# Kernel optimization log

Hardware: AMD Instinct MI355X
Metric: run time of the kernel (lower is better)

The kernel has to match this reference:

```python
import jax, jax.numpy as jnp
import numpy as np
from math import sqrt

B, TS_D, SEG, D, H = 16, 2, 1024, 256, 8
D_FF = 1024
DK = D // H
EPS = 1e-5


def _layernorm(x, g, b):
    mu = jnp.mean(x, axis=-1, keepdims=True)
    var = jnp.mean(jnp.square(x - mu), axis=-1, keepdims=True)
    return (x - mu) * jax.lax.rsqrt(var + EPS) * g + b


def setup_inputs() -> dict:
    key = jax.random.key(0)
    ks = jax.random.split(key, 16)
    s = 0.02
    return {
        "x": jax.random.normal(ks[0], (B, TS_D, SEG, D), dtype=jnp.float32),
        "Wq": jax.random.normal(ks[1], (D, D), dtype=jnp.float32) * s,
        "bq": jnp.zeros((D,), jnp.float32),
        "Wk": jax.random.normal(ks[2], (D, D), dtype=jnp.float32) * s,
        "bk": jnp.zeros((D,), jnp.float32),
        "Wv": jax.random.normal(ks[3], (D, D), dtype=jnp.float32) * s,
        "bv": jnp.zeros((D,), jnp.float32),
        "Wo": jax.random.normal(ks[4], (D, D), dtype=jnp.float32) * s,
        "bo": jnp.zeros((D,), jnp.float32),
        "g31": jnp.ones((D,), jnp.float32),
        "b31": jnp.zeros((D,), jnp.float32),
        "W1": jax.random.normal(ks[5], (D, D_FF), dtype=jnp.float32) * s,
        "b1": jnp.zeros((D_FF,), jnp.float32),
        "W2": jax.random.normal(ks[6], (D_FF, D), dtype=jnp.float32) * s,
        "b2": jnp.zeros((D,), jnp.float32),
        "g41": jnp.ones((D,), jnp.float32),
        "b41": jnp.zeros((D,), jnp.float32),
    }


def reference(x, Wq, bq, Wk, bk, Wv, bv, Wo, bo, g31, b31, W1, b1, W2, b2, g41, b41):
    # x: [B, ts_d=2, seg, d]; output is final_out2 (only live path of the module)
    b, ts_d, seg, d = x.shape
    scale = 1.0 / sqrt(DK)
    segments = x.reshape(b, ts_d * seg, d)            # [B, 2*seg, d]
    Q = (segments @ Wq + bq).reshape(b, -1, H, DK)
    K = (segments @ Wk + bk).reshape(b, -1, H, DK)
    V = (segments @ Wv + bv).reshape(b, -1, H, DK)
    q = Q[:, :seg]       # first seg positions (channel 0)
    k = K[:, -seg:]      # last seg positions (channel 1)
    v = V[:, -seg:]
    # cross-segment dual attention
    A1 = jax.nn.softmax(scale * jnp.einsum('blhe,bshe->bhls', q, k), axis=-1)
    out1 = jnp.einsum('bhls,bshd->blhd', A1, v).reshape(b, seg, d)
    A2 = jax.nn.softmax(scale * jnp.einsum('blhe,bshe->bhls', k, q), axis=-1)
    out2 = jnp.einsum('bhls,bshd->blhd', A2, q).reshape(b, seg, d)
    y = jnp.concatenate([out1, out2], axis=1) @ Wo + bo   # [B, 2*seg, d]
    h = _layernorm(segments + y, g31, b31)
    mlp = jax.nn.gelu(h @ W1 + b1, approximate=False) @ W2 + b2
    h = _layernorm(h + mlp, g41, b41)
    return h.reshape(b, ts_d, seg, d)
```

## Files before the change

kernel.cpp:

```cpp
#include <hip/hip_runtime.h>
#include <hip/hip_bf16.h>
#include <math.h>

#define BATCH 16
#define SEG 1024
#define DMODEL 256
#define NH 8
#define DK 32
#define DFF 1024
#define NTOK (BATCH * 2 * SEG)
#define EPS 1e-5f

typedef __attribute__((ext_vector_type(8))) short short8;
typedef __attribute__((ext_vector_type(4))) short short4b;
typedef __attribute__((ext_vector_type(4))) float f32x4;

#if __has_builtin(__builtin_amdgcn_exp2f)
#define EXP2(x) __builtin_amdgcn_exp2f(x)
#else
#define EXP2(x) __expf((x) * 0.6931471805599453f)
#endif

__device__ __forceinline__ ushort f2bf(float x) {
    union { float f; unsigned u; } a; a.f = x;
    unsigned r = a.u + 0x7fffu + ((a.u >> 16) & 1u);
    return (ushort)(r >> 16);
}

typedef const __attribute__((address_space(1))) unsigned gas_u32;
typedef __attribute__((address_space(3))) unsigned las_u32;
__device__ __forceinline__ void gload_lds16(const ushort* g, ushort* l) {
    __builtin_amdgcn_global_load_lds((gas_u32*)g, (las_u32*)l, 16, 0, 0);
}

__global__ __launch_bounds__(256) void wfrag_kernel(
    const float* __restrict__ src, ushort* __restrict__ dst, int K, int N, int order)
{
    const int tid = blockIdx.x * 256 + threadIdx.x;
    const int KT_ = K >> 5, NT_ = N >> 4;
    const int total = KT_ * NT_ * 64;
    if (tid >= total) return;
    const int lane = tid & 63;
    const int frag = tid >> 6;
    int kt, nt;
    if (order) { kt = frag / NT_; nt = frag % NT_; }
    else       { nt = frag / KT_; kt = frag % KT_; }
    const int quad = lane >> 4, l = lane & 15;
    const float* s = src + (size_t)(kt * 32 + quad * 8) * N + nt * 16 + l;
    short8 v;
#pragma unroll
    for (int j = 0; j < 8; j++) v[j] = (short)f2bf(s[(size_t)j * N]);
    *(short8*)&dst[(size_t)tid * 8] = v;
}

#define ASTR 264

__device__ __forceinline__ void dense256_pass(
    const ushort* __restrict__ Wf, ushort* WL, const short8* af,
    f32x4* acc, int t, int w, int lane)
{
#pragma unroll
    for (int nt = 0; nt < 16; ++nt) acc[nt] = (f32x4){0.f, 0.f, 0.f, 0.f};
    {
        const ushort* g = Wf + (size_t)w * 4096 + lane * 8;
        ushort* ld = WL + w * 4096;
#pragma unroll
        for (int i = 0; i < 8; ++i) gload_lds16(g + i * 512, ld + i * 512);
    }
    __syncthreads();
    for (int c = 0; c < 4; ++c) {
        if (c < 3) {
            const ushort* g = Wf + (size_t)(c + 1) * 16384 + w * 4096 + lane * 8;
            ushort* ld = WL + ((c + 1) & 1) * 8192 + w * 4096;
#pragma unroll
            for (int i = 0; i < 8; ++i) gload_lds16(g + i * 512, ld + i * 512);
        }
        const ushort* buf = WL + (c & 1) * 8192;
#pragma unroll
        for (int n2 = 0; n2 < 4; ++n2)
#pragma unroll
            for (int kt = 0; kt < 8; ++kt) {
                const short8 bf_ = *(const short8*)&buf[(n2 * 8 + kt) * 512 + lane * 8];
                acc[c * 4 + n2] = __builtin_amdgcn_mfma_f32_16x16x32_bf16(af[kt], bf_, acc[c * 4 + n2], 0, 0, 0);
            }
        __syncthreads();
    }
}

__global__ __launch_bounds__(256) void qkv_mfma_kernel(
    const float* __restrict__ x,
    const ushort* __restrict__ Wqf, const float* __restrict__ bq,
    const ushort* __restrict__ Wkf, const float* __restrict__ bk,
    const ushort* __restrict__ Wvf, const float* __restrict__ bv,
    ushort* __restrict__ qbuf, ushort* __restrict__ kbuf,
    ushort* __restrict__ qt, ushort* __restrict__ vt)
{
    __shared__ __align__(16) ushort SM[64 * ASTR];
    const int bid = blockIdx.x;
    const int which = bid >> 8;
    const int sub = bid & 255;
    const int b = sub >> 4, ti = sub & 15;
    const int half = (which == 0) ? 0 : 1;
    const int t = threadIdx.x;
    const int w = t >> 6, lane = t & 63, l = lane & 15, quad = lane >> 4;

    const float* xrow = x + ((size_t)b * 2048 + (size_t)half * 1024 + ti * 64) * 256;
#pragma unroll
    for (int p = 0; p < 16; ++p) {
        int ch = t + 256 * p;
        int row = ch >> 6, c4 = ch & 63;
        float4 v = *(const float4*)&xrow[row * 256 + c4 * 4];
        uint2 pk;
        pk.x = (unsigned)f2bf(v.x) | ((unsigned)f2bf(v.y) << 16);
        pk.y = (unsigned)f2bf(v.z) | ((unsigned)f2bf(v.w) << 16);
        *(uint2*)&SM[row * ASTR + c4 * 4] = pk;
    }
    __syncthreads();

    short8 af[8];
#pragma unroll
    for (int kt = 0; kt < 8; ++kt)
        af[kt] = *(const short8*)&SM[(w * 16 + l) * ASTR + kt * 32 + quad * 8];
    __syncthreads();

    const ushort* Wf  = (which == 0) ? Wqf : (which == 1 ? Wkf : Wvf);
    const float* bias = (which == 0) ? bq  : (which == 1 ? bk  : bv);
    const float kscale = (which == 1) ? 0.25503472f : 1.0f;

    f32x4 acc[16];
    dense256_pass(Wf, SM, af, acc, t, w, lane);

    ushort bfv[16][4];
#pragma unroll
    for (int nt = 0; nt < 16; ++nt) {
        const float bb = bias[nt * 16 + l];
#pragma unroll
        for (int r = 0; r < 4; ++r) bfv[nt][r] = f2bf((acc[nt][r] + bb) * kscale);
    }

    if (which <= 1) {
        ushort* obuf = which ? kbuf : qbuf;
#pragma unroll
        for (int nt = 0; nt < 16; ++nt) {
            const int h = nt >> 1, e = (nt & 1) * 16 + l;
#pragma unroll
            for (int r = 0; r < 4; ++r) {
                int tok = ti * 64 + w * 16 + quad * 4 + r;
                obuf[(((size_t)b * 8 + h) * SEG + tok) * 32 + e] = bfv[nt][r];
            }
        }
    }
    if (which != 1) {
        ushort* tb = which ? vt : qt;
#pragma unroll
        for (int nt = 0; nt < 16; ++nt)
#pragma unroll
            for (int r = 0; r < 4; ++r)
                SM[(nt * 16 + l) * 66 + w * 16 + quad * 4 + r] = bfv[nt][r];
        __syncthreads();
        const int d = t, hh = t >> 5, e = t & 31;
        ushort* dr = tb + (((size_t)b * 8 + hh) * 32 + e) * 1024 + ti * 64;
#pragma unroll
        for (int j = 0; j < 8; ++j) {
            uint2 v;
            v.x = *(const unsigned*)&SM[d * 66 + j * 8];
            v.y = *(const unsigned*)&SM[d * 66 + j * 8 + 2];
            unsigned z0 = *(const unsigned*)&SM[d * 66 + j * 8 + 4];
            unsigned z1 = *(const unsigned*)&SM[d * 66 + j * 8 + 6];
            *(uint4*)&dr[j * 8] = make_uint4(v.x, v.y, z0, z1);
        }
    }
}

#define KTILE 128
#define KP 40
#define VP 132

__global__ __launch_bounds__(256) void attn_mfma_kernel(
    const ushort* __restrict__ qbuf, const ushort* __restrict__ kbuf,
    const ushort* __restrict__ qt, const ushort* __restrict__ vt,
    ushort* __restrict__ abuf)
{
    __shared__ __align__(16) ushort Kl[KTILE * KP];
    __shared__ __align__(16) ushort Vl[32 * VP];

    const int bid   = blockIdx.x;
    const int sbh   = bid & 255;
    const int qtile = bid >> 8;
    const int stage = sbh >> 7;
    const int b     = (sbh >> 3) & 15;
    const int h     = sbh & 7;

    const ushort* Qm = stage ? kbuf : qbuf;
    const ushort* Km = stage ? qbuf : kbuf;
    const ushort* Vt = stage ? qt : vt;
    const size_t bh = ((size_t)b * 8 + h) * SEG * 32;

    const int t    = threadIdx.x;
    const int w    = t >> 6;
    const int lane = t & 63;
    const int l    = lane & 15;
    const int quad = lane >> 4;

    const int qrow = qtile * 64 + w * 16 + l;
    const short8 qf = *(const short8*)&Qm[bh + (size_t)qrow * 32 + quad * 8];

    f32x4 o0 = {0.f, 0.f, 0.f, 0.f};
    f32x4 o1 = {0.f, 0.f, 0.f, 0.f};
    f32x4 o2 = {0.f, 0.f, 0.f, 0.f};
    const short4b ones = {(short)0x3F80, (short)0x3F80, (short)0x3F80, (short)0x3F80};

    for (int tile = 0; tile < 8; ++tile) {
        __syncthreads();
        const ushort* Kg = &Km[bh + (size_t)(tile * KTILE) * 32];
#pragma unroll
        for (int p = 0; p < 2; ++p) {
            int ch = t + 256 * p;
            int row = ((ch >> 6) << 4) | (ch & 15);
            int part = (ch >> 4) & 3;
            *(short8*)&Kl[row * KP + part * 8] = *(const short8*)&Kg[row * 32 + part * 8];
        }
        const ushort* Vg = &Vt[bh + (size_t)tile * KTILE];
#pragma unroll
        for (int p = 0; p < 2; ++p) {
            int ch = t + 256 * p;
            int d = ch >> 4, c = ch & 15;
            *(short8*)&Vl[d * VP + c * 8] = *(const short8*)&Vg[(size_t)d * 1024 + c * 8];
        }
        __syncthreads();

#pragma unroll
        for (int kb = 0; kb < 8; ++kb) {
            const short8 kf = *(const short8*)&Kl[(kb * 16 + l) * KP + quad * 8];
            f32x4 z = {0.f, 0.f, 0.f, 0.f};
            f32x4 sc = __builtin_amdgcn_mfma_f32_16x16x32_bf16(kf, qf, z, 0, 0, 0);
            union { float f; unsigned u; } a0, a1, a2, a3;
            a0.f = EXP2(sc[0]); a1.f = EXP2(sc[1]);
            a2.f = EXP2(sc[2]); a3.f = EXP2(sc[3]);
            unsigned lo = __builtin_amdgcn_perm(a1.u, a0.u, 0x07060302u);
            unsigned hi = __builtin_amdgcn_perm(a3.u, a2.u, 0x07060302u);
            union { uint2 u; short4b s; } pk; pk.u = make_uint2(lo, hi);
            const short4b vf0 = *(const short4b*)&Vl[l * VP + kb * 16 + quad * 4];
            const short4b vf1 = *(const short4b*)&Vl[(16 + l) * VP + kb * 16 + quad * 4];
            o0 = __builtin_amdgcn_mfma_f32_16x16x16bf16_1k(vf0, pk.s, o0, 0, 0, 0);
            o1 = __builtin_amdgcn_mfma_f32_16x16x16bf16_1k(vf1, pk.s, o1, 0, 0, 0);
            o2 = __builtin_amdgcn_mfma_f32_16x16x16bf16_1k(ones, pk.s, o2, 0, 0, 0);
        }
    }

    const float inv = 1.0f / o2[0];
#pragma unroll
    for (int r = 0; r < 4; ++r) { o0[r] *= inv; o1[r] *= inv; }

    __syncthreads();
    ushort* Ob = &Kl[w * 16 * 40];
#pragma unroll
    for (int r = 0; r < 4; ++r) {
        Ob[l * 40 + quad * 4 + r]      = f2bf(o0[r]);
        Ob[l * 40 + 16 + quad * 4 + r] = f2bf(o1[r]);
    }
    __syncthreads();
    const int q = lane >> 2, part = lane & 3;
    const short8 ov = *(const short8*)&Ob[q * 40 + part * 8];
    const int tok = qtile * 64 + w * 16 + q;
    *(short8*)&abuf[((size_t)b * 2 * SEG + (size_t)stage * SEG + tok) * 256 + h * 32 + part * 8] = ov;
}

__global__ __launch_bounds__(256) void proj_mfma_kernel(
    const ushort* __restrict__ abuf, const ushort* __restrict__ Wof,
    const float* __restrict__ bo, const float* __restrict__ x,
    const float* __restrict__ g31, const float* __restrict__ b31,
    float* __restrict__ hout)
{
    __shared__ __align__(16) ushort SM[64 * ASTR];
    const int bid = blockIdx.x;
    const size_t tok0 = (size_t)bid * 64;
    const int t = threadIdx.x;
    const int w = t >> 6, lane = t & 63, l = lane & 15, quad = lane >> 4;

#pragma unroll
    for (int p = 0; p < 8; ++p) {
        int ch = t + 256 * p;
        int row = ch >> 5, c8 = ch & 31;
        *(short8*)&SM[row * ASTR + c8 * 8] = *(const short8*)&abuf[(tok0 + row) * 256 + c8 * 8];
    }
    __syncthreads();

    short8 af[8];
#pragma unroll
    for (int kt = 0; kt < 8; ++kt)
        af[kt] = *(const short8*)&SM[(w * 16 + l) * ASTR + kt * 32 + quad * 8];
    __syncthreads();

    f32x4 acc[16];
    dense256_pass(Wof, SM, af, acc, t, w, lane);

#pragma unroll
    for (int nt = 0; nt < 16; ++nt) {
        const int d = nt * 16 + l;
        const float bv = bo[d];
#pragma unroll
        for (int r = 0; r < 4; ++r) {
            size_t tok = tok0 + w * 16 + quad * 4 + r;
            acc[nt][r] += bv + x[tok * 256 + d];
        }
    }

    float mu_[4], is_[4];
#pragma unroll
    for (int r = 0; r < 4; ++r) {
        float s = 0.f;
#pragma unroll
        for (int nt = 0; nt < 16; ++nt) s += acc[nt][r];
        s += __shfl_xor(s, 1); s += __shfl_xor(s, 2);
        s += __shfl_xor(s, 4); s += __shfl_xor(s, 8);
        float mu = s * (1.0f / 256.0f);
        float vs = 0.f;
#pragma unroll
        for (int nt = 0; nt < 16; ++nt) { float dd = acc[nt][r] - mu; vs += dd * dd; }
        vs += __shfl_xor(vs, 1); vs += __shfl_xor(vs, 2);
        vs += __shfl_xor(vs, 4); vs += __shfl_xor(vs, 8);
        mu_[r] = mu;
        is_[r] = rsqrtf(vs * (1.0f / 256.0f) + EPS);
    }

#pragma unroll
    for (int nt = 0; nt < 16; ++nt) {
        const int d = nt * 16 + l;
        const float gg = g31[d], bb = b31[d];
#pragma unroll
        for (int r = 0; r < 4; ++r) {
            size_t tok = tok0 + w * 16 + quad * 4 + r;
            hout[tok * 256 + d] = (acc[nt][r] - mu_[r]) * is_[r] * gg + bb;
        }
    }
}

#define GP 40

__global__ __launch_bounds__(256, 2) void mlp_mfma_kernel(
    const float* __restrict__ W1dummy_unused, const ushort* __restrict__ W1f,
    const float* __restrict__ b1, const ushort* __restrict__ W2f,
    const float* __restrict__ b2, const float* __restrict__ g41,
    const float* __restrict__ b41, float* __restrict__ io)
{
    __shared__ __align__(16) ushort SM[2 * 16384];
    __shared__ __align__(16) ushort G[64 * GP];
    __shared__ __align__(16) float B1L[DFF];
    __shared__ float PS[2][2][64];
    const int bid = blockIdx.x;
    const size_t tok0 = (size_t)bid * 64;
    const int t = threadIdx.x;
    const int w = t >> 6, lane = t & 63, l = lane & 15, quad = lane >> 4;
    const int g = w >> 1, f = w & 1;

    const float* hrow = io + tok0 * 256;
#pragma unroll
    for (int p = 0; p < 16; ++p) {
        int ch = t + 256 * p;
        int row = ch >> 6, c4 = ch & 63;
        float4 v = *(const float4*)&hrow[row * 256 + c4 * 4];
        uint2 pk;
        pk.x = (unsigned)f2bf(v.x) | ((unsigned)f2bf(v.y) << 16);
        pk.y = (unsigned)f2bf(v.z) | ((unsigned)f2bf(v.w) << 16);
        *(uint2*)&SM[row * ASTR + c4 * 4] = pk;
    }
    *(float4*)&B1L[t * 4] = *(const float4*)&b1[t * 4];
    __syncthreads();

    short8 af[2][8];
#pragma unroll
    for (int j = 0; j < 2; ++j)
#pragma unroll
        for (int kt = 0; kt < 8; ++kt)
            af[j][kt] = *(const short8*)&SM[(g * 32 + j * 16 + l) * ASTR + kt * 32 + quad * 8];
    __syncthreads();

    f32x4 out[2][8];
#pragma unroll
    for (int j = 0; j < 2; ++j)
#pragma unroll
        for (int nt = 0; nt < 8; ++nt) out[j][nt] = (f32x4){0.f, 0.f, 0.f, 0.f};

    {
        const ushort* g1 = W1f + w * 2048 + lane * 8;
        const ushort* g2 = W2f + w * 2048 + lane * 8;
        ushort* l1 = SM + w * 2048;
        ushort* l2 = SM + 8192 + w * 2048;
#pragma unroll
        for (int i = 0; i < 4; ++i) {
            gload_lds16(g1 + i * 512, l1 + i * 512);
            gload_lds16(g2 + i * 512, l2 + i * 512);
        }
    }
    __syncthreads();

    for (int c = 0; c < 32; ++c) {
        if (c < 31) {
            const int nb = (c + 1) & 1;
            const ushort* g1 = W1f + (size_t)(c + 1) * 8192 + w * 2048 + lane * 8;
            ushort* l1 = SM + nb * 16384 + w * 2048;
            const ushort* g2 = W2f + (size_t)(c + 1) * 8192 + w * 2048 + lane * 8;
            ushort* l2 = SM + nb * 16384 + 8192 + w * 2048;
#pragma unroll
            for (int i = 0; i < 4; ++i) {
                gload_lds16(g1 + i * 512, l1 + i * 512);
                gload_lds16(g2 + i * 512, l2 + i * 512);
            }
        }
        const ushort* WL = SM + (c & 1) * 16384;

        f32x4 s0 = {0.f, 0.f, 0.f, 0.f};
        f32x4 s1 = {0.f, 0.f, 0.f, 0.f};
#pragma unroll
        for (int kt = 0; kt < 8; ++kt) {
            const short8 bf_ = *(const short8*)&WL[(f * 8 + kt) * 512 + lane * 8];
            s0 = __builtin_amdgcn_mfma_f32_16x16x32_bf16(af[0][kt], bf_, s0, 0, 0, 0);
            s1 = __builtin_amdgcn_mfma_f32_16x16x32_bf16(af[1][kt], bf_, s1, 0, 0, 0);
        }

        const float bv = B1L[c * 32 + f * 16 + l];
#pragma unroll
        for (int j = 0; j < 2; ++j) {
#pragma unroll
            for (int r = 0; r < 4; ++r) {
                float v = (j ? s1[r] : s0[r]) + bv;
                float au = fabsf(v) * 0.70710678118654752f;
                float t1 = __builtin_amdgcn_rcpf(fmaf(0.3275911f, au, 1.0f));
                float e  = EXP2(au * au * -1.4426950408889634f);
                float p5 = fmaf(fmaf(fmaf(fmaf(1.061405429f, t1, -1.453152027f),
                                t1, 1.421413741f), t1, -0.284496736f), t1, 0.254829592f) * t1;
                float erf_abs = fmaf(-p5, e, 1.0f);
                float gl = fmaf(0.5f * fabsf(v), erf_abs, 0.5f * v);
                G[(g * 32 + j * 16 + quad * 4 + r) * GP + f * 16 + l] = f2bf(gl);
            }
        }
        __syncthreads();

        const short8 gf0 = *(const short8*)&G[(g * 32 + l) * GP + quad * 8];
        const short8 gf1 = *(const short8*)&G[(g * 32 + 16 + l) * GP + quad * 8];
#pragma unroll
        for (int nt = 0; nt < 8; ++nt) {
            const short8 bf_ = *(const short8*)&WL[8192 + (f * 8 + nt) * 512 + lane * 8];
            out[0][nt] = __builtin_amdgcn_mfma_f32_16x16x32_bf16(gf0, bf_, out[0][nt], 0, 0, 0);
            out[1][nt] = __builtin_amdgcn_mfma_f32_16x16x32_bf16(gf1, bf_, out[1][nt], 0, 0, 0);
        }
        __syncthreads();
    }

#pragma unroll
    for (int j = 0; j < 2; ++j)
#pragma unroll
        for (int nt = 0; nt < 8; ++nt) {
            const int d = f * 128 + nt * 16 + l;
            const float bvv = b2[d];
#pragma unroll
            for (int r = 0; r < 4; ++r) {
                size_t tok = tok0 + g * 32 + j * 16 + quad * 4 + r;
                out[j][nt][r] += bvv + io[tok * 256 + d];
            }
        }

#pragma unroll
    for (int j = 0; j < 2; ++j)
#pragma unroll
        for (int r = 0; r < 4; ++r) {
            float p1 = 0.f, p2 = 0.f;
#pragma unroll
            for (int nt = 0; nt < 8; ++nt) { float v = out[j][nt][r]; p1 += v; p2 += v * v; }
            p1 += __shfl_xor(p1, 1); p1 += __shfl_xor(p1, 2);
            p1 += __shfl_xor(p1, 4); p1 += __shfl_xor(p1, 8);
            p2 += __shfl_xor(p2, 1); p2 += __shfl_xor(p2, 2);
            p2 += __shfl_xor(p2, 4); p2 += __shfl_xor(p2, 8);
            if (l == 0) {
                PS[0][f][g * 32 + j * 16 + quad * 4 + r] = p1;
                PS[1][f][g * 32 + j * 16 + quad * 4 + r] = p2;
            }
        }
    __syncthreads();

    float mu_[2][4], is_[2][4];
#pragma unroll
    for (int j = 0; j < 2; ++j)
#pragma unroll
        for (int r = 0; r < 4; ++r) {
            int tk = g * 32 + j * 16 + quad * 4 + r;
            float S1 = PS[0][0][tk] + PS[0][1][tk];
            float S2 = PS[1][0][tk] + PS[1][1][tk];
            float mu = S1 * (1.0f / 256.0f);
            float var = S2 * (1.0f / 256.0f) - mu * mu;
            mu_[j][r] = mu;
            is_[j][r] = rsqrtf(var + EPS);
        }

#pragma unroll
    for (int j = 0; j < 2; ++j)
#pragma unroll
        for (int nt = 0; nt < 8; ++nt) {
            const int d = f * 128 + nt * 16 + l;
            const float gg = g41[d], bb = b41[d];
#pragma unroll
            for (int r = 0; r < 4; ++r) {
                size_t tok = tok0 + g * 32 + j * 16 + quad * 4 + r;
                io[tok * 256 + d] = (out[j][nt][r] - mu_[j][r]) * is_[j][r] * gg + bb;
            }
        }
}

extern "C" void kernel_launch(void* const* d_in, const int* in_sizes, int n_in,
                              void* d_out, int out_size, void* d_ws, size_t ws_size,
                              hipStream_t stream)
{
    const float* x   = (const float*)d_in[0];
    const float* Wq  = (const float*)d_in[1];
    const float* bq  = (const float*)d_in[2];
    const float* Wk  = (const float*)d_in[3];
    const float* bk  = (const float*)d_in[4];
    const float* Wv  = (const float*)d_in[5];
    const float* bv  = (const float*)d_in[6];
    const float* Wo  = (const float*)d_in[7];
    const float* bo  = (const float*)d_in[8];
    const float* g31 = (const float*)d_in[9];
    const float* b31 = (const float*)d_in[10];
    const float* W1  = (const float*)d_in[11];
    const float* b1  = (const float*)d_in[12];
    const float* W2  = (const float*)d_in[13];
    const float* b2  = (const float*)d_in[14];
    const float* g41 = (const float*)d_in[15];
    const float* b41 = (const float*)d_in[16];

    float* out = (float*)d_out;

    const size_t HALF = (size_t)BATCH * SEG * DMODEL;
    ushort* qbuf = (ushort*)d_ws;
    ushort* kbuf = qbuf + HALF;
    ushort* qt   = kbuf + HALF;
    ushort* vt   = qt + HALF;
    ushort* abuf = vt + HALF;
    ushort* Wqf  = abuf + 2 * HALF;
    ushort* Wkf  = Wqf + 65536;
    ushort* Wvf  = Wkf + 65536;
    ushort* Wof  = Wvf + 65536;
    ushort* W1f  = Wof + 65536;
    ushort* W2f  = W1f + 262144;

    wfrag_kernel<<<32, 256, 0, stream>>>(Wq, Wqf, 256, 256, 0);
    wfrag_kernel<<<32, 256, 0, stream>>>(Wk, Wkf, 256, 256, 0);
    wfrag_kernel<<<32, 256, 0, stream>>>(Wv, Wvf, 256, 256, 0);
    wfrag_kernel<<<32, 256, 0, stream>>>(Wo, Wof, 256, 256, 0);
    wfrag_kernel<<<128, 256, 0, stream>>>(W1, W1f, 256, 1024, 0);
    wfrag_kernel<<<128, 256, 0, stream>>>(W2, W2f, 1024, 256, 1);

    qkv_mfma_kernel<<<768, 256, 0, stream>>>(x, Wqf, bq, Wkf, bk, Wvf, bv,
                                             qbuf, kbuf, qt, vt);
    attn_mfma_kernel<<<2 * BATCH * NH * (SEG / 64), 256, 0, stream>>>(qbuf, kbuf, qt, vt, abuf);
    proj_mfma_kernel<<<NTOK / 64, 256, 0, stream>>>(abuf, Wof, bo, x, g31, b31, out);
    mlp_mfma_kernel<<<NTOK / 64, 256, 0, stream>>>(nullptr, W1f, b1, W2f, b2, g41, b41, out);
}
```

Baseline: 283.8 us.

## Double MLP block tile to 128 tokens with 512 threads sharing weight chunks

The fused MLP kernel now processes 128 tokens per block with 8 waves instead of 64 tokens with 4 waves. Each streamed W1/W2 chunk in LDS is therefore reused by twice as many tokens, halving global weight traffic per token, and each thread issues half as many async copies. The input rows are staged in two 64-row halves through the shared buffer to keep LDS usage within budget. The trade-offs are half as many blocks, which means fewer blocks to fill the GPU, a larger LDS footprint per block that may limit occupancy, and an epilogue that must correctly handle the larger PS and G arrays (only partly visible here).

After: 291.2 us. 1.03x slower.

```diff
diff --git a/kernel.cpp b/kernel.cpp
--- a/kernel.cpp
+++ b/kernel.cpp
@@ -338,75 +338,94 @@
 
 #define GP 40
 
-__global__ __launch_bounds__(256, 2) void mlp_mfma_kernel(
+__global__ __launch_bounds__(512, 2) void mlp_mfma_kernel(
     const float* __restrict__ W1dummy_unused, const ushort* __restrict__ W1f,
     const float* __restrict__ b1, const ushort* __restrict__ W2f,
     const float* __restrict__ b2, const float* __restrict__ g41,
     const float* __restrict__ b41, float* __restrict__ io)
 {
     __shared__ __align__(16) ushort SM[2 * 16384];
-    __shared__ __align__(16) ushort G[64 * GP];
+    __shared__ __align__(16) ushort G[128 * GP];
     __shared__ __align__(16) float B1L[DFF];
-    __shared__ float PS[2][2][64];
+    __shared__ float PS[2][2][128];
     const int bid = blockIdx.x;
-    const size_t tok0 = (size_t)bid * 64;
+    const size_t tok0 = (size_t)bid * 128;
     const int t = threadIdx.x;
     const int w = t >> 6, lane = t & 63, l = lane & 15, quad = lane >> 4;
-    const int g = w >> 1, f = w & 1;
-
-    const float* hrow = io + tok0 * 256;
-#pragma unroll
-    for (int p = 0; p < 16; ++p) {
-        int ch = t + 256 * p;
-        int row = ch >> 6, c4 = ch & 63;
-        float4 v = *(const float4*)&hrow[row * 256 + c4 * 4];
-        uint2 pk;
-        pk.x = (unsigned)f2bf(v.x) | ((unsigned)f2bf(v.y) << 16);
-        pk.y = (unsigned)f2bf(v.z) | ((unsigned)f2bf(v.w) << 16);
-        *(uint2*)&SM[row * ASTR + c4 * 4] = pk;
-    }
-    *(float4*)&B1L[t * 4] = *(const float4*)&b1[t * 4];
-    __syncthreads();
+    const int g = w & 3, f = w >> 2;
 
     short8 af[2][8];
+    {
+        const float* hrow = io + tok0 * 256;
+#pragma unroll
+        for (int p = 0; p < 8; ++p) {
+            int ch = t + 512 * p;
+            int row = ch >> 6, c4 = ch & 63;
+            float4 v = *(const float4*)&hrow[row * 256 + c4 * 4];
+            uint2 pk;
+            pk.x = (unsigned)f2bf(v.x) | ((unsigned)f2bf(v.y) << 16);
+            pk.y = (unsigned)f2bf(v.z) | ((unsigned)f2bf(v.w) << 16);
+            *(uint2*)&SM[row * ASTR + c4 * 4] = pk;
+        }
+        *(float2*)&B1L[t * 2] = *(const float2*)&b1[t * 2];
+    }
+    __syncthreads();
+    if (g < 2) {
+#pragma unroll
+        for (int j = 0; j < 2; ++j)
+#pragma unroll
+            for (int kt = 0; kt < 8; ++kt)
+                af[j][kt] = *(const short8*)&SM[(g * 32 + j * 16 + l) * ASTR + kt * 32 + quad * 8];
+    }
+    __syncthreads();
+    {
+        const float* hrow = io + (tok0 + 64) * 256;
+#pragma unroll
+        for (int p = 0; p < 8; ++p) {
+            int ch = t + 512 * p;
+            int row = ch >> 6, c4 = ch & 63;
+            float4 v = *(const float4*)&hrow[row * 256 + c4 * 4];
+            uint2 pk;
+            pk.x = (unsigned)f2bf(v.x) | ((unsigned)f2bf(v.y) << 16);
+            pk.y = (unsigned)f2bf(v.z) | ((unsigned)f2bf(v.w) << 16);
+            *(uint2*)&SM[row * ASTR + c4 * 4] = pk;
+        }
+    }
+    __syncthreads();
+    if (g >= 2) {
+#pragma unroll
+        for (int j = 0; j < 2; ++j)
+#pragma unroll
+            for (int kt = 0; kt < 8; ++kt)
+                af[j][kt] = *(const short8*)&SM[((g - 2) * 32 + j * 16 + l) * ASTR + kt * 32 + quad * 8];
+    }
+    __syncthreads();
+
+    f32x4 out[2][8];
 #pragma unroll
     for (int j = 0; j < 2; ++j)
 #pragma unroll
-        for (int kt = 0; kt < 8; ++kt)
-            af[j][kt] = *(const short8*)&SM[(g * 32 + j * 16 + l) * ASTR + kt * 32 + quad * 8];
-    __syncthreads();
-
-    f32x4 out[2][8];
-#pragma unroll
-    for (int j = 0; j < 2; ++j)
-#pragma unroll
         for (int nt = 0; nt < 8; ++nt) out[j][nt] = (f32x4){0.f, 0.f, 0.f, 0.f};
 
     {
-        const ushort* g1 = W1f + w * 2048 + lane * 8;
-        const ushort* g2 = W2f + w * 2048 + lane * 8;
-        ushort* l1 = SM + w * 2048;
-        ushort* l2 = SM + 8192 + w * 2048;
-#pragma unroll
-        for (int i = 0; i < 4; ++i) {
-            gload_lds16(g1 + i * 512, l1 + i * 512);
-            gload_lds16(g2 + i * 512, l2 + i * 512);
-        }
+        const ushort* g1 = W1f + w * 1024 + lane * 8;
+        const ushort* g2 = W2f + w * 1024 + lane * 8;
+        ushort* l1 = SM + w * 1024;
+        ushort* l2 = SM + 8192 + w * 1024;
+        gload_lds16(g1, l1); gload_lds16(g1 + 512, l1 + 512);
+        gload_lds16(g2, l2); gload_lds16(g2 + 512, l2 + 512);
     }
     __syncthreads();
 
     for (int c = 0; c < 32; ++c) {
         if (c < 31) {
             const int nb = (c + 1) & 1;
-            const ushort* g1 = W1f + (size_t)(c + 1) * 8192 + w * 2048 + lane * 8;
-            ushort* l1 = SM + nb * 16384 + w * 2048;
-            const ushort* g2 = W2f + (size_t)(c + 1) * 8192 + w * 2048 + lane * 8;
-            ushort* l2 = SM + nb * 16384 + 8192 + w * 2048;
-#pragma unroll
-            for (int i = 0; i < 4; ++i) {
-                gload_lds16(g1 + i * 512, l1 + i * 512);
-                gload_lds16(g2 + i * 512, l2 + i * 512);
-            }
+            const ushort* g1 = W1f + (size_t)(c + 1) * 8192 + w * 1024 + lane * 8;
+            ushort* l1 = SM + nb * 16384 + w * 1024;
+            const ushort* g2 = W2f + (size_t)(c + 1) * 8192 + w * 1024 + lane * 8;
+            ushort* l2 = SM + nb * 16384 + 8192 + w * 1024;
+            gload_lds16(g1, l1); gload_lds16(g1 + 512, l1 + 512);
+            gload_lds16(g2, l2); gload_lds16(g2 + 512, l2 + 512);
         }
         const ushort* WL = SM + (c & 1) * 16384;
 
@@ -555,5 +574,5 @@
                                              qbuf, kbuf, qt, vt);
     attn_mfma_kernel<<<2 * BATCH * NH * (SEG / 64), 256, 0, stream>>>(qbuf, kbuf, qt, vt, abuf);
     proj_mfma_kernel<<<NTOK / 64, 256, 0, stream>>>(abuf, Wof, bo, x, g31, b31, out);
-    mlp_mfma_kernel<<<NTOK / 64, 256, 0, stream>>>(nullptr, W1f, b1, W2f, b2, g41, b41, out);
-}
+    mlp_mfma_kernel<<<NTOK / 128, 512, 0, stream>>>(nullptr, W1f, b1, W2f, b2, g41, b41, out);
+}
```

## Merge weight-fragment launches and register-prefetch next K/V tile in attention

Applied to the files above, without the earlier changes.

Combines six weight-conversion kernel launches into one kernel that dispatches on block index, cutting launch overhead. In the attention kernel, the next K/V tile is loaded from global memory into registers while the current tile is being computed, so load latency overlaps with MFMA work instead of stalling between barriers. This costs extra registers for the prefetch buffers, which could lower occupancy.

Result: faster. 270.3 us (-4.7%).

```diff
diff --git a/kernel.cpp b/kernel.cpp
--- a/kernel.cpp
+++ b/kernel.cpp
@@ -33,13 +33,24 @@
     __builtin_amdgcn_global_load_lds((gas_u32*)g, (las_u32*)l, 16, 0, 0);
 }
 
-__global__ __launch_bounds__(256) void wfrag_kernel(
-    const float* __restrict__ src, ushort* __restrict__ dst, int K, int N, int order)
-{
-    const int tid = blockIdx.x * 256 + threadIdx.x;
+__global__ __launch_bounds__(256) void wfrag_all_kernel(
+    const float* __restrict__ Wq, const float* __restrict__ Wk,
+    const float* __restrict__ Wv, const float* __restrict__ Wo,
+    const float* __restrict__ W1, const float* __restrict__ W2,
+    ushort* __restrict__ Wqf, ushort* __restrict__ Wkf,
+    ushort* __restrict__ Wvf, ushort* __restrict__ Wof,
+    ushort* __restrict__ W1f, ushort* __restrict__ W2f)
+{
+    const int blk = blockIdx.x;
+    const float* src; ushort* dst; int K, N, order, base;
+    if (blk < 32)       { src = Wq; dst = Wqf; K = 256;  N = 256;  order = 0; base = 0;   }
+    else if (blk < 64)  { src = Wk; dst = Wkf; K = 256;  N = 256;  order = 0; base = 32;  }
+    else if (blk < 96)  { src = Wv; dst = Wvf; K = 256;  N = 256;  order = 0; base = 64;  }
+    else if (blk < 128) { src = Wo; dst = Wof; K = 256;  N = 256;  order = 0; base = 96;  }
+    else if (blk < 256) { src = W1; dst = W1f; K = 256;  N = 1024; order = 0; base = 128; }
+    else                { src = W2; dst = W2f; K = 1024; N = 256;  order = 1; base = 256; }
+    const int tid = (blk - base) * 256 + threadIdx.x;
     const int KT_ = K >> 5, NT_ = N >> 4;
-    const int total = KT_ * NT_ * 64;
-    if (tid >= total) return;
     const int lane = tid & 63;
     const int frag = tid >> 6;
     int kt, nt;
@@ -210,24 +221,35 @@
     f32x4 o2 = {0.f, 0.f, 0.f, 0.f};
     const short4b ones = {(short)0x3F80, (short)0x3F80, (short)0x3F80, (short)0x3F80};
 
+    const int ch0 = t, ch1 = t + 256;
+    const int kr0 = ((ch0 >> 6) << 4) | (ch0 & 15), kp0 = (ch0 >> 4) & 3;
+    const int kr1 = ((ch1 >> 6) << 4) | (ch1 & 15), kp1 = (ch1 >> 4) & 3;
+    const int vd0 = ch0 >> 4, vc0 = ch0 & 15;
+    const int vd1 = ch1 >> 4, vc1 = ch1 & 15;
+    const ushort* Kgb = &Km[bh];
+    const ushort* Vgb = &Vt[bh];
+
+    short8 rk0 = *(const short8*)&Kgb[(size_t)kr0 * 32 + kp0 * 8];
+    short8 rk1 = *(const short8*)&Kgb[(size_t)kr1 * 32 + kp1 * 8];
+    short8 rv0 = *(const short8*)&Vgb[(size_t)vd0 * 1024 + vc0 * 8];
+    short8 rv1 = *(const short8*)&Vgb[(size_t)vd1 * 1024 + vc1 * 8];
+
     for (int tile = 0; tile < 8; ++tile) {
         __syncthreads();
-        const ushort* Kg = &Km[bh + (size_t)(tile * KTILE) * 32];
-#pragma unroll
-        for (int p = 0; p < 2; ++p) {
-            int ch = t + 256 * p;
-            int row = ((ch >> 6) << 4) | (ch & 15);
-            int part = (ch >> 4) & 3;
-            *(short8*)&Kl[row * KP + part * 8] = *(const short8*)&Kg[row * 32 + part * 8];
-        }
-        const ushort* Vg = &Vt[bh + (size_t)tile * KTILE];
-#pragma unroll
-        for (int p = 0; p < 2; ++p) {
-            int ch = t + 256 * p;
-            int d = ch >> 4, c = ch & 15;
-            *(short8*)&Vl[d * VP + c * 8] = *(const short8*)&Vg[(size_t)d * 1024 + c * 8];
-        }
+        *(short8*)&Kl[kr0 * KP + kp0 * 8] = rk0;
+        *(short8*)&Kl[kr1 * KP + kp1 * 8] = rk1;
+        *(short8*)&Vl[vd0 * VP + vc0 * 8] = rv0;
+        *(short8*)&Vl[vd1 * VP + vc1 * 8] = rv1;
         __syncthreads();
+
+        if (tile < 7) {
+            const size_t ko = (size_t)(tile + 1) * KTILE * 32;
+            const size_t vo = (size_t)(tile + 1) * KTILE;
+            rk0 = *(const short8*)&Kgb[ko + (size_t)kr0 * 32 + kp0 * 8];
+            rk1 = *(const short8*)&Kgb[ko + (size_t)kr1 * 32 + kp1 * 8];
+            rv0 = *(const short8*)&Vgb[vo + (size_t)vd0 * 1024 + vc0 * 8];
+            rv1 = *(const short8*)&Vgb[vo + (size_t)vd1 * 1024 + vc1 * 8];
+        }
 
 #pragma unroll
         for (int kb = 0; kb < 8; ++kb) {
@@ -544,12 +566,8 @@
     ushort* W1f  = Wof + 65536;
     ushort* W2f  = W1f + 262144;
 
-    wfrag_kernel<<<32, 256, 0, stream>>>(Wq, Wqf, 256, 256, 0);
-    wfrag_kernel<<<32, 256, 0, stream>>>(Wk, Wkf, 256, 256, 0);
-    wfrag_kernel<<<32, 256, 0, stream>>>(Wv, Wvf, 256, 256, 0);
-    wfrag_kernel<<<32, 256, 0, stream>>>(Wo, Wof, 256, 256, 0);
-    wfrag_kernel<<<128, 256, 0, stream>>>(W1, W1f, 256, 1024, 0);
-    wfrag_kernel<<<128, 256, 0, stream>>>(W2, W2f, 1024, 256, 1);
+    wfrag_all_kernel<<<384, 256, 0, stream>>>(Wq, Wk, Wv, Wo, W1, W2,
+                                              Wqf, Wkf, Wvf, Wof, W1f, W2f);
 
     qkv_mfma_kernel<<<768, 256, 0, stream>>>(x, Wqf, bq, Wkf, bk, Wvf, bv,
                                              qbuf, kbuf, qt, vt);
```
